# Performance work log

Hardware: AMD Instinct MI355X
Metric: run time of the kernel (lower is better)

The kernel has to match this reference:

```python
import jax, jax.numpy as jnp
from jax import lax
import numpy as np

B, C_IN, C_OUT, H, W, K = 4, 128, 256, 64, 64, 3
KK = K * K
MID = C_IN // 4
EPS = 1e-5


def conv2d(x, w, b, pad, groups=1):
    out = lax.conv_general_dilated(x, w, (1, 1), [(pad, pad), (pad, pad)],
                                   feature_group_count=groups,
                                   dimension_numbers=('NCHW', 'OIHW', 'NCHW'))
    return out + b[None, :, None, None]


def bnorm(x, g, b, m, v):
    # inference-mode BatchNorm2d
    scale = (g / jnp.sqrt(v + EPS))
    return (x - m[None, :, None, None]) * scale[None, :, None, None] + b[None, :, None, None]


def bilinear_gather(x, py, px):
    # x: (B,C,H,W); py/px: (B,KK,H,W) float sample coords; zero outside bounds
    Bb, C, Hh, Ww = x.shape
    xf = x.reshape(Bb, C, Hh * Ww)
    y0 = jnp.floor(py)
    x0 = jnp.floor(px)
    wy1 = py - y0
    wx1 = px - x0

    def corner(yc, xc, wgt):
        valid = (yc >= 0) & (yc <= Hh - 1) & (xc >= 0) & (xc <= Ww - 1)
        yi = jnp.clip(yc, 0, Hh - 1).astype(jnp.int32)
        xi = jnp.clip(xc, 0, Ww - 1).astype(jnp.int32)
        idx = (yi * Ww + xi).reshape(Bb, -1)  # (B, KK*H*W)
        g = jax.vmap(lambda f, i: f[:, i])(xf, idx).reshape(Bb, C, *py.shape[1:])
        return g * (wgt * valid)[:, None]

    return (corner(y0, x0, (1 - wy1) * (1 - wx1))
            + corner(y0, x0 + 1, (1 - wy1) * wx1)
            + corner(y0 + 1, x0, wy1 * (1 - wx1))
            + corner(y0 + 1, x0 + 1, wy1 * wx1))


def deform_conv2d(x, offset, mask, w, b, pad=1):
    # modulated deformable conv v2, stride=1, dilation=1, groups=1, dg=1
    Bb, C, Hh, Ww = x.shape
    off = offset.reshape(Bb, KK, 2, Hh, Ww)  # (dy,dx) per kernel point
    k = jnp.arange(KK)
    ky = (k // K).astype(x.dtype)
    kx = (k % K).astype(x.dtype)
    py = (jnp.arange(Hh, dtype=x.dtype) - pad)[None, None, :, None] + ky[None, :, None, None] + off[:, :, 0]
    px = (jnp.arange(Ww, dtype=x.dtype) - pad)[None, None, None, :] + kx[None, :, None, None] + off[:, :, 1]
    val = bilinear_gather(x, py, px) * mask[:, None]  # (B,C,KK,H,W)
    return jnp.einsum('bckhw,ock->bohw', val, w.reshape(w.shape[0], C, KK)) + b[None, :, None, None]


def setup_inputs() -> dict:
    key = jax.random.key(0)
    ks = iter(jax.random.split(key, 40))

    def P(shape, scale=0.05):
        return jax.random.normal(next(ks), shape, jnp.float32) * scale

    d = {}
    d['x'] = jax.random.normal(next(ks), (B, C_IN, H, W), jnp.float32)
    # DCConv offset branch
    d['oc1_w'] = P((MID, C_IN, 3, 3)); d['oc1_b'] = P((MID,))
    d['obn_g'] = jnp.ones((MID,)); d['obn_b'] = jnp.zeros((MID,))
    d['obn_m'] = jnp.zeros((MID,)); d['obn_v'] = jnp.ones((MID,))
    d['oc2_w'] = P((2 * KK, MID, 3, 3), 0.01); d['oc2_b'] = P((2 * KK,), 0.01)
    # DCConv mask branch
    d['mc1_w'] = P((MID, C_IN, 3, 3)); d['mc1_b'] = P((MID,))
    d['mbn_g'] = jnp.ones((MID,)); d['mbn_b'] = jnp.zeros((MID,))
    d['mbn_m'] = jnp.zeros((MID,)); d['mbn_v'] = jnp.ones((MID,))
    d['mc2_w'] = P((KK, MID, 3, 3), 0.01); d['mc2_b'] = jnp.ones((KK,))
    # DCConv main weight
    d['dc_w'] = P((C_OUT, C_IN, 3, 3)); d['dc_b'] = jnp.zeros((C_OUT,))
    # contour branch: depthwise 3x3 + BN + ReLU + 1x1
    d['cb_dw_w'] = P((C_IN, 1, 3, 3)); d['cb_dw_b'] = P((C_IN,))
    d['cbn_g'] = jnp.ones((C_IN,)); d['cbn_b'] = jnp.zeros((C_IN,))
    d['cbn_m'] = jnp.zeros((C_IN,)); d['cbn_v'] = jnp.ones((C_IN,))
    d['cb_pw_w'] = P((C_OUT // 2, C_IN, 1, 1)); d['cb_pw_b'] = P((C_OUT // 2,))
    # spatial attention 7x7 -> 1 channel
    d['sa_w'] = P((1, C_OUT + C_OUT // 2, 7, 7)); d['sa_b'] = jnp.zeros((1,))
    # fusion 1x1 + BN + ReLU
    d['fu_w'] = P((C_OUT, C_OUT + C_OUT // 2, 1, 1)); d['fu_b'] = jnp.zeros((C_OUT,))
    d['fbn_g'] = jnp.ones((C_OUT,)); d['fbn_b'] = jnp.zeros((C_OUT,))
    d['fbn_m'] = jnp.zeros((C_OUT,)); d['fbn_v'] = jnp.ones((C_OUT,))
    return d


def reference(x, oc1_w, oc1_b, obn_g, obn_b, obn_m, obn_v, oc2_w, oc2_b,
              mc1_w, mc1_b, mbn_g, mbn_b, mbn_m, mbn_v, mc2_w, mc2_b,
              dc_w, dc_b, cb_dw_w, cb_dw_b, cbn_g, cbn_b, cbn_m, cbn_v,
              cb_pw_w, cb_pw_b, sa_w, sa_b, fu_w, fu_b, fbn_g, fbn_b, fbn_m, fbn_v):
    # DCConv: offsets + sigmoid masks + modulated deformable conv
    h = jax.nn.relu(bnorm(conv2d(x, oc1_w, oc1_b, 1), obn_g, obn_b, obn_m, obn_v))
    offset = conv2d(h, oc2_w, oc2_b, 1)
    hm = jax.nn.relu(bnorm(conv2d(x, mc1_w, mc1_b, 1), mbn_g, mbn_b, mbn_m, mbn_v))
    mask = jax.nn.sigmoid(conv2d(hm, mc2_w, mc2_b, 1))
    main_feat = deform_conv2d(x, offset, mask, dc_w, dc_b, pad=1)
    # contour branch
    hc = jax.nn.relu(bnorm(conv2d(x, cb_dw_w, cb_dw_b, 1, groups=C_IN), cbn_g, cbn_b, cbn_m, cbn_v))
    contour_feat = conv2d(hc, cb_pw_w, cb_pw_b, 0)
    combined = jnp.concatenate([main_feat, contour_feat], axis=1)
    attn = jax.nn.sigmoid(conv2d(combined, sa_w, sa_b, 3))
    combined = combined * attn
    return jax.nn.relu(bnorm(conv2d(combined, fu_w, fu_b, 0), fbn_g, fbn_b, fbn_m, fbn_v))
```

## Files before the change

### kernel.cpp

```cpp
#include <hip/hip_runtime.h>
#include <hip/hip_bf16.h>
#include <math.h>

#define BN   4
#define CIN  128
#define COUT 256
#define HWP  4096

typedef __hip_bfloat16 bf16;
typedef __attribute__((ext_vector_type(8))) short sh8;
typedef __attribute__((ext_vector_type(4))) float f32x4;

__device__ __forceinline__ float b2f(bf16 v) { return __bfloat162float(v); }
__device__ __forceinline__ float bflo(unsigned u) { return __uint_as_float(u << 16); }
__device__ __forceinline__ float bfhi(unsigned u) { return __uint_as_float(u & 0xffff0000u); }
__device__ __forceinline__ unsigned short f2bfbits(float f) {
    union { bf16 h; unsigned short u; } cv; cv.h = __float2bfloat16(f); return cv.u;
}
__device__ __forceinline__ float bfj(const uint4& c, int j) {
    unsigned u = (&c.x)[j >> 1];
    return (j & 1) ? bfhi(u) : bflo(u);
}

__global__ __launch_bounds__(256) void transpose_x_kernel(const float* __restrict__ x,
                                                          bf16* __restrict__ xt)
{
    __shared__ bf16 t[64][136];
    const int b = blockIdx.x >> 6, chunk = blockIdx.x & 63;
    const int pos0 = chunk * 64;
    const int tid = threadIdx.x;
    const int lane = tid & 63, wv = tid >> 6;
    const float* xb = x + (size_t)b * CIN * HWP + pos0 + lane;
    #pragma unroll 4
    for (int j = 0; j < 32; j++) {
        int ci = wv * 32 + j;
        t[lane][ci] = __float2bfloat16(xb[(size_t)ci * HWP]);
    }
    __syncthreads();
    const int p = tid >> 2, cig = tid & 3;
    uint4* dst = (uint4*)(xt + ((size_t)b * HWP + pos0 + p) * 128 + cig * 32);
    const uint4* src = (const uint4*)&t[p][cig * 32];
    #pragma unroll
    for (int q = 0; q < 4; q++) dst[q] = src[q];
}

__global__ __launch_bounds__(256) void prep_wBf_kernel(const float* __restrict__ w,
                                                       bf16* __restrict__ wBf) {
    int o = blockIdx.x * 256 + threadIdx.x;
    if (o >= 256 * 1152) return;
    int j = o & 7, o2 = o >> 3;
    int lane = o2 & 63, t = o2 >> 6;
    int l16 = lane & 15, quad = lane >> 4;
    int mt = t & 3, t2 = t >> 2;
    int kt = t2 % 36, wv = t2 / 36;
    int co = wv * 64 + mt * 16 + l16;
    int kk = kt * 32 + quad * 8 + j;
    int k = kk >> 7, ci = kk & 127;
    wBf[o] = __float2bfloat16(w[co * 1152 + ci * 9 + k]);
}

__global__ __launch_bounds__(256) void prep_conv1_kernel(
    const float* __restrict__ oc1_w, const float* __restrict__ oc1_b,
    const float* __restrict__ obn_g, const float* __restrict__ obn_b,
    const float* __restrict__ obn_m, const float* __restrict__ obn_v,
    const float* __restrict__ mc1_w, const float* __restrict__ mc1_b,
    const float* __restrict__ mbn_g, const float* __restrict__ mbn_b,
    const float* __restrict__ mbn_m, const float* __restrict__ mbn_v,
    bf16* __restrict__ wCf, float* __restrict__ ab)
{
    int o = blockIdx.x * 256 + threadIdx.x;
    if (o < 64 * 1152) {
        int j = o & 7, o2 = o >> 3;
        int lane = o2 & 63, t = o2 >> 6;
        int l16 = lane & 15, quad = lane >> 4;
        int kt = t % 36, wv = t / 36;
        int co = wv * 16 + l16;
        int kk = kt * 32 + quad * 8 + j;
        int k = kk >> 7, ci = kk & 127;
        float v = (co < 32) ? oc1_w[co * 1152 + ci * 9 + k]
                            : mc1_w[(co - 32) * 1152 + ci * 9 + k];
        wCf[o] = __float2bfloat16(v);
    } else if (o < 64 * 1152 + 64) {
        int c = o - 64 * 1152;
        float g, bb, m, vv, bias;
        if (c < 32) { g = obn_g[c]; bb = obn_b[c]; m = obn_m[c]; vv = obn_v[c]; bias = oc1_b[c]; }
        else { int c2 = c - 32; g = mbn_g[c2]; bb = mbn_b[c2]; m = mbn_m[c2]; vv = mbn_v[c2]; bias = mc1_b[c2]; }
        float alpha = g / sqrtf(vv + 1e-5f);
        ab[c] = alpha;
        ab[64 + c] = (bias - m) * alpha + bb;
    }
}

__global__ __launch_bounds__(256) void prep_fuse_kernel(
    const float* __restrict__ fu_w, const float* __restrict__ fu_b,
    const float* __restrict__ fbn_g, const float* __restrict__ fbn_b,
    const float* __restrict__ fbn_m, const float* __restrict__ fbn_v,
    const float* __restrict__ sa_w,
    bf16* __restrict__ wFf, bf16* __restrict__ wSAf, float* __restrict__ fab)
{
    int o = blockIdx.x * 256 + threadIdx.x;
    if (o < 98304) {
        int j = o & 7, o2 = o >> 3;
        int lane = o2 & 63, t = o2 >> 6;
        int l16 = lane & 15, quad = lane >> 4;
        int mt = t & 3, t2 = t >> 2;
        int kt = t2 % 12, wv = t2 / 12;
        int co = wv * 64 + mt * 16 + l16;
        int kk = kt * 32 + quad * 8 + j;
        wFf[o] = __float2bfloat16(fu_w[co * 384 + kk]);
    } else if (o < 98304 + 24576) {
        int idx = o - 98304;
        int j = idx & 7, o2 = idx >> 3;
        int lane = o2 & 63, t = o2 >> 6;
        int l16 = lane & 15, quad = lane >> 4;
        int kt = t % 12, wv = t / 12;
        int jr = wv * 16 + l16;
        int kk = kt * 32 + quad * 8 + j;
        wSAf[idx] = (jr < 49) ? __float2bfloat16(sa_w[kk * 49 + jr]) : __float2bfloat16(0.f);
    } else if (o < 98304 + 24576 + 256) {
        int co = o - 98304 - 24576;
        float alpha = fbn_g[co] / sqrtf(fbn_v[co] + 1e-5f);
        fab[co] = alpha;
        fab[256 + co] = (fu_b[co] - fbn_m[co]) * alpha + fbn_b[co];
    }
}

__global__ __launch_bounds__(256) void prep_misc_kernel(
    const float* __restrict__ oc2_w, const float* __restrict__ mc2_w,
    const float* __restrict__ cb_pw_w,
    const float* __restrict__ cb_dw_b, const float* __restrict__ cbn_g,
    const float* __restrict__ cbn_b, const float* __restrict__ cbn_m,
    const float* __restrict__ cbn_v,
    bf16* __restrict__ wDf, bf16* __restrict__ wPf, float* __restrict__ dwab)
{
    int o = blockIdx.x * 256 + threadIdx.x;
    if (o < 18432) {
        int j = o & 7, o2 = o >> 3;
        int lane = o2 & 63, t = o2 >> 6;
        int l16 = lane & 15, quad = lane >> 4;
        int mt = t & 1, kt = t >> 1;
        int co = mt * 16 + l16;
        int kk = kt * 32 + quad * 8 + j;
        int k = kk >> 6, c = kk & 63;
        float v = 0.f;
        if (co < 18 && c < 32) v = oc2_w[co * 288 + c * 9 + k];
        else if (co >= 18 && co < 27 && c >= 32) v = mc2_w[(co - 18) * 288 + (c - 32) * 9 + k];
        wDf[o] = __float2bfloat16(v);
    } else if (o < 18432 + 16384) {
        int idx = o - 18432;
        int j = idx & 7, o2 = idx >> 3;
        int lane = o2 & 63, t = o2 >> 6;
        int l16 = lane & 15, quad = lane >> 4;
        int wv = t >> 3, kt = (t >> 1) & 3, mt = t & 1;
        int co = wv * 32 + mt * 16 + l16;
        int kk = kt * 32 + quad * 8 + j;
        wPf[idx] = __float2bfloat16(cb_pw_w[co * 128 + kk]);
    } else if (o < 18432 + 16384 + 128) {
        int c = o - 18432 - 16384;
        float alpha = cbn_g[c] / sqrtf(cbn_v[c] + 1e-5f);
        dwab[c] = alpha;
        dwab[128 + c] = (cb_dw_b[c] - cbn_m[c]) * alpha + cbn_b[c];
    }
}

__global__ __launch_bounds__(256) void conv1_mfma_kernel(
    const bf16* __restrict__ xt, const bf16* __restrict__ wCf, const float* __restrict__ ab,
    bf16* __restrict__ ht)
{
    __shared__ __align__(16) bf16 val[16][1160];

    const int bid = blockIdx.x;
    const int b = (bid & 7) >> 1;
    const int tile = ((bid >> 3) << 1) | (bid & 1);
    const int pos0 = tile * 16;
    const int y = tile >> 2, x0 = (tile & 3) * 16;
    const int tid = threadIdx.x;
    const int cig = tid & 15, pix = tid >> 4;
    const int ci0 = cig * 8;
    const int xxp = x0 + pix;

    const bf16* xtb = xt + (size_t)b * HWP * 128;
    #pragma unroll
    for (int k = 0; k < 9; k++) {
        int yy = y + k / 3 - 1, xx = xxp + k % 3 - 1;
        bool valid = (yy >= 0 && yy <= 63 && xx >= 0 && xx <= 63);
        uint4 c = {0, 0, 0, 0};
        if (valid) c = *(const uint4*)(xtb + (size_t)(yy * 64 + xx) * 128 + ci0);
        *(uint4*)&val[pix][k * 128 + ci0] = c;
    }
    __syncthreads();

    const int lane = tid & 63, wv = tid >> 6;
    const int quad = lane >> 4, l16 = lane & 15;
    f32x4 acc = {0, 0, 0, 0};
    const bf16* wl0 = wCf + (size_t)wv * 36 * 512 + lane * 8;
    const bf16* vbase = &val[l16][quad * 8];

    sh8 af = *(const sh8*)(wl0);
    sh8 bf = *(const sh8*)(vbase);
    sh8 afn, bfn;
    for (int kt = 0; kt < 36; kt++) {
        if (kt < 35) {
            afn = *(const sh8*)(wl0 + (kt + 1) * 512);
            bfn = *(const sh8*)(vbase + (kt + 1) * 32);
        }
        acc = __builtin_amdgcn_mfma_f32_16x16x32_bf16(af, bf, acc, 0, 0, 0);
        af = afn; bf = bfn;
    }

    float o0 = fmaxf(acc[0] * ab[wv * 16 + quad * 4 + 0] + ab[64 + wv * 16 + quad * 4 + 0], 0.f);
    float o1 = fmaxf(acc[1] * ab[wv * 16 + quad * 4 + 1] + ab[64 + wv * 16 + quad * 4 + 1], 0.f);
    float o2 = fmaxf(acc[2] * ab[wv * 16 + quad * 4 + 2] + ab[64 + wv * 16 + quad * 4 + 2], 0.f);
    float o3 = fmaxf(acc[3] * ab[wv * 16 + quad * 4 + 3] + ab[64 + wv * 16 + quad * 4 + 3], 0.f);
    uint2 pk;
    pk.x = (unsigned)f2bfbits(o0) | ((unsigned)f2bfbits(o1) << 16);
    pk.y = (unsigned)f2bfbits(o2) | ((unsigned)f2bfbits(o3) << 16);
    *(uint2*)(ht + ((size_t)b * HWP + pos0 + l16) * 64 + wv * 16 + quad * 4) = pk;
}

__global__ __launch_bounds__(256) void conv2_mfma_kernel(
    const bf16* __restrict__ ht, const bf16* __restrict__ wDf,
    const float* __restrict__ oc2_b, const float* __restrict__ mc2_b,
    float* __restrict__ offsb, float* __restrict__ mskb)
{
    __shared__ __align__(16) bf16 val[32][584];

    const int bid = blockIdx.x;
    const int b = bid >> 7, tile = bid & 127;
    const int y = tile >> 1, x0 = (tile & 1) * 32;
    const int tid = threadIdx.x;

    {
        const int cig = tid & 7, pix = tid >> 3;
        const int xxp = x0 + pix;
        const bf16* hb = ht + (size_t)b * HWP * 64;
        #pragma unroll
        for (int k = 0; k < 9; k++) {
            int yy = y + k / 3 - 1, xx = xxp + k % 3 - 1;
            bool valid = (yy >= 0 && yy <= 63 && xx >= 0 && xx <= 63);
            uint4 c = {0, 0, 0, 0};
            if (valid) c = *(const uint4*)(hb + (size_t)(yy * 64 + xx) * 64 + cig * 8);
            *(uint4*)&val[pix][k * 64 + cig * 8] = c;
        }
    }
    __syncthreads();

    const int lane = tid & 63, wv = tid >> 6;
    const int quad = lane >> 4, l16 = lane & 15;
    const int ph = wv >> 1, mt = wv & 1;
    f32x4 acc = {0, 0, 0, 0};
    const bf16* wl0 = wDf + ((size_t)mt * 64 + lane) * 8;
    const bf16* vbase = &val[ph * 16 + l16][quad * 8];

    sh8 af = *(const sh8*)(wl0);
    sh8 bf = *(const sh8*)(vbase);
    sh8 afn, bfn;
    for (int kt = 0; kt < 18; kt++) {
        if (kt < 17) {
            afn = *(const sh8*)(wl0 + (kt + 1) * 1024);
            bfn = *(const sh8*)(vbase + (kt + 1) * 32);
        }
        acc = __builtin_amdgcn_mfma_f32_16x16x32_bf16(af, bf, acc, 0, 0, 0);
        af = afn; bf = bfn;
    }

    const int pos = y * 64 + x0 + ph * 16 + l16;
    #pragma unroll
    for (int r = 0; r < 4; r++) {
        int co = mt * 16 + quad * 4 + r;
        if (co < 18) {
            offsb[(size_t)(b * 18 + co) * HWP + pos] = acc[r] + oc2_b[co];
        } else if (co < 27) {
            float s = acc[r] + mc2_b[co - 18];
            mskb[(size_t)(b * 9 + (co - 18)) * HWP + pos] = 1.f / (1.f + expf(-s));
        }
    }
}

__global__ __launch_bounds__(256) void dwconv_px_kernel(
    const bf16* __restrict__ xt, const float* __restrict__ dw_w, const float* __restrict__ dwab,
    bf16* __restrict__ htc)
{
    __shared__ float wl[1152];
    __shared__ float abl[256];
    const int bid = blockIdx.x;
    const int b = bid >> 8, tile = bid & 255;
    const int y = tile >> 2, x0 = (tile & 3) * 16;
    const int tid = threadIdx.x;
    for (int i = tid; i < 1152; i += 256) wl[i] = dw_w[i];
    if (tid < 256) abl[tid] = dwab[tid];
    __syncthreads();

    const int cig = tid & 15, pix = tid >> 4;
    const int ci0 = cig * 8;
    const int xxp = x0 + pix;
    const bf16* xtb = xt + (size_t)b * HWP * 128;

    float g[8] = {0, 0, 0, 0, 0, 0, 0, 0};
    #pragma unroll
    for (int k = 0; k < 9; k++) {
        int yy = y + k / 3 - 1, xx = xxp + k % 3 - 1;
        if (yy < 0 || yy > 63 || xx < 0 || xx > 63) continue;
        uint4 c = *(const uint4*)(xtb + (size_t)(yy * 64 + xx) * 128 + ci0);
        #pragma unroll
        for (int j = 0; j < 8; j++)
            g[j] += wl[(ci0 + j) * 9 + k] * bfj(c, j);
    }
    float o[8];
    #pragma unroll
    for (int j = 0; j < 8; j++)
        o[j] = fmaxf(g[j] * abl[ci0 + j] + abl[128 + ci0 + j], 0.f);
    uint4 pk;
    pk.x = (unsigned)f2bfbits(o[0]) | ((unsigned)f2bfbits(o[1]) << 16);
    pk.y = (unsigned)f2bfbits(o[2]) | ((unsigned)f2bfbits(o[3]) << 16);
    pk.z = (unsigned)f2bfbits(o[4]) | ((unsigned)f2bfbits(o[5]) << 16);
    pk.w = (unsigned)f2bfbits(o[6]) | ((unsigned)f2bfbits(o[7]) << 16);
    *(uint4*)(htc + ((size_t)b * HWP + y * 64 + xxp) * 128 + ci0) = pk;
}

__global__ __launch_bounds__(256) void pw_mfma_kernel(
    const bf16* __restrict__ htc, const bf16* __restrict__ wPf, const float* __restrict__ bias,
    bf16* __restrict__ combined)
{
    const int bid = blockIdx.x;
    const int b = bid >> 8, tile = bid & 255;
    const int pos0 = tile * 16;
    const int tid = threadIdx.x;
    const int lane = tid & 63, wv = tid >> 6;
    const int quad = lane >> 4, l16 = lane & 15;

    f32x4 acc[2] = {f32x4{0,0,0,0}, f32x4{0,0,0,0}};
    const bf16* fb = htc + ((size_t)b * HWP + pos0 + l16) * 128 + quad * 8;
    const bf16* wl0 = wPf + (size_t)wv * 4096 + lane * 8;
    for (int kt = 0; kt < 4; kt++) {
        sh8 bf = *(const sh8*)(fb + kt * 32);
        #pragma unroll
        for (int mt = 0; mt < 2; mt++) {
            sh8 af = *(const sh8*)(wl0 + (kt * 2 + mt) * 512);
            acc[mt] = __builtin_amdgcn_mfma_f32_16x16x32_bf16(af, bf, acc[mt], 0, 0, 0);
        }
    }

    bf16* ct = combined + ((size_t)b * HWP + pos0 + l16) * 384 + 256;
    #pragma unroll
    for (int mt = 0; mt < 2; mt++) {
        int co_b = wv * 32 + mt * 16 + quad * 4;
        uint2 pk;
        pk.x = (unsigned)f2bfbits(acc[mt][0] + bias[co_b])     | ((unsigned)f2bfbits(acc[mt][1] + bias[co_b + 1]) << 16);
        pk.y = (unsigned)f2bfbits(acc[mt][2] + bias[co_b + 2]) | ((unsigned)f2bfbits(acc[mt][3] + bias[co_b + 3]) << 16);
        *(uint2*)(ct + co_b) = pk;
    }
}

__global__ __launch_bounds__(256) void deform_kernel(
    const bf16* __restrict__ xt, const float* __restrict__ offs, const float* __restrict__ msk,
    const bf16* __restrict__ wBf, const float* __restrict__ bias, bf16* __restrict__ combined)
{
    __shared__ __align__(16) bf16 val[16][1160];
    __shared__ int   ti[144][4];
    __shared__ float tw[144][4];

    const int bid = blockIdx.x;
    const int b = (bid & 7) >> 1;
    const int tile = ((bid >> 3) << 1) | (bid & 1);
    const int pos0 = tile * 16;
    const int tid = threadIdx.x;

    if (tid < 144) {
        int k = tid >> 4, pix = tid & 15;
        int pos = pos0 + pix;
        int y = pos >> 6, xc = pos & 63;
        float offy = offs[(size_t)(b * 18 + 2 * k) * HWP + pos];
        float offx = offs[(size_t)(b * 18 + 2 * k + 1) * HWP + pos];
        float m = msk[(size_t)(b * 9 + k) * HWP + pos];
        float py = (float)(y - 1 + k / 3) + offy;
        float px = (float)(xc - 1 + k % 3) + offx;
        float fy = floorf(py), fx = floorf(px);
        float wy1 = py - fy, wx1 = px - fx;
        int y0 = (int)fy, x0 = (int)fx;
        int y1 = y0 + 1, x1 = x0 + 1;
        bool vy0 = (y0 >= 0 && y0 <= 63), vy1 = (y1 >= 0 && y1 <= 63);
        bool vx0 = (x0 >= 0 && x0 <= 63), vx1 = (x1 >= 0 && x1 <= 63);
        int cy0 = min(max(y0, 0), 63), cy1 = min(max(y1, 0), 63);
        int cx0 = min(max(x0, 0), 63), cx1 = min(max(x1, 0), 63);
        ti[tid][0] = cy0 * 64 + cx0;  tw[tid][0] = (vy0 && vx0) ? (1.f - wy1) * (1.f - wx1) * m : 0.f;
        ti[tid][1] = cy0 * 64 + cx1;  tw[tid][1] = (vy0 && vx1) ? (1.f - wy1) * wx1 * m : 0.f;
        ti[tid][2] = cy1 * 64 + cx0;  tw[tid][2] = (vy1 && vx0) ? wy1 * (1.f - wx1) * m : 0.f;
        ti[tid][3] = cy1 * 64 + cx1;  tw[tid][3] = (vy1 && vx1) ? wy1 * wx1 * m : 0.f;
    }
    __syncthreads();

    {
        const int cig = tid & 15, pix = tid >> 4;
        const int ci0 = cig * 8;
        const bf16* xtb = xt + (size_t)b * HWP * 128;
        for (int k = 0; k < 9; k++) {
            const int e = k * 16 + pix;
            const int i0 = ti[e][0], i1 = ti[e][1], i2 = ti[e][2], i3 = ti[e][3];
            const float w0 = tw[e][0], w1 = tw[e][1], w2 = tw[e][2], w3 = tw[e][3];
            uint4 c0 = *(const uint4*)(xtb + (size_t)i0 * 128 + ci0);
            uint4 c1 = *(const uint4*)(xtb + (size_t)i1 * 128 + ci0);
            uint4 c2 = *(const uint4*)(xtb + (size_t)i2 * 128 + ci0);
            uint4 c3 = *(const uint4*)(xtb + (size_t)i3 * 128 + ci0);
            float g[8];
            #pragma unroll
            for (int j = 0; j < 8; j++)
                g[j] = w0 * bfj(c0, j) + w1 * bfj(c1, j) + w2 * bfj(c2, j) + w3 * bfj(c3, j);
            uint4 pk;
            pk.x = (unsigned)f2bfbits(g[0]) | ((unsigned)f2bfbits(g[1]) << 16);
            pk.y = (unsigned)f2bfbits(g[2]) | ((unsigned)f2bfbits(g[3]) << 16);
            pk.z = (unsigned)f2bfbits(g[4]) | ((unsigned)f2bfbits(g[5]) << 16);
            pk.w = (unsigned)f2bfbits(g[6]) | ((unsigned)f2bfbits(g[7]) << 16);
            *(uint4*)&val[pix][k * 128 + ci0] = pk;
        }
    }
    __syncthreads();

    const int lane = tid & 63, wv = tid >> 6;
    const int quad = lane >> 4, l16 = lane & 15;
    f32x4 acc[4] = {f32x4{0,0,0,0}, f32x4{0,0,0,0}, f32x4{0,0,0,0}, f32x4{0,0,0,0}};

    const bf16* wl0 = wBf + (size_t)wv * 73728 + lane * 8;
    const bf16* vbase = &val[l16][quad * 8];

    sh8 af[4], afn[4], bf, bfn;
    bf = *(const sh8*)(vbase);
    #pragma unroll
    for (int mt = 0; mt < 4; mt++) af[mt] = *(const sh8*)(wl0 + mt * 512);
    for (int kt = 0; kt < 36; kt++) {
        if (kt < 35) {
            bfn = *(const sh8*)(vbase + (kt + 1) * 32);
            #pragma unroll
            for (int mt = 0; mt < 4; mt++)
                afn[mt] = *(const sh8*)(wl0 + ((kt + 1) * 4 + mt) * 512);
        }
        #pragma unroll
        for (int mt = 0; mt < 4; mt++)
            acc[mt] = __builtin_amdgcn_mfma_f32_16x16x32_bf16(af[mt], bf, acc[mt], 0, 0, 0);
        bf = bfn;
        #pragma unroll
        for (int mt = 0; mt < 4; mt++) af[mt] = afn[mt];
    }

    bf16* ct = combined + ((size_t)b * HWP + pos0 + l16) * 384;
    #pragma unroll
    for (int mt = 0; mt < 4; mt++) {
        int co_b = wv * 64 + mt * 16 + quad * 4;
        uint2 pk;
        pk.x = (unsigned)f2bfbits(acc[mt][0] + bias[co_b])     | ((unsigned)f2bfbits(acc[mt][1] + bias[co_b + 1]) << 16);
        pk.y = (unsigned)f2bfbits(acc[mt][2] + bias[co_b + 2]) | ((unsigned)f2bfbits(acc[mt][3] + bias[co_b + 3]) << 16);
        *(uint2*)(ct + co_b) = pk;
    }
}

__global__ __launch_bounds__(256) void sa_gemm_kernel(
    const bf16* __restrict__ combined, const bf16* __restrict__ wSAf, float* __restrict__ part)
{
    const int bid = blockIdx.x;
    const int b = bid >> 8, tile = bid & 255;
    const int pos0 = tile * 16;
    const int tid = threadIdx.x;
    const int lane = tid & 63, wv = tid >> 6;
    const int quad = lane >> 4, l16 = lane & 15;

    f32x4 acc = {0, 0, 0, 0};
    const bf16* fb = combined + ((size_t)b * HWP + pos0 + l16) * 384 + quad * 8;
    const bf16* wl0 = wSAf + (size_t)wv * 6144 + lane * 8;

    sh8 af = *(const sh8*)(wl0);
    sh8 bf = *(const sh8*)(fb);
    sh8 afn, bfn;
    for (int kt = 0; kt < 12; kt++) {
        if (kt < 11) {
            afn = *(const sh8*)(wl0 + (kt + 1) * 512);
            bfn = *(const sh8*)(fb + (kt + 1) * 32);
        }
        acc = __builtin_amdgcn_mfma_f32_16x16x32_bf16(af, bf, acc, 0, 0, 0);
        af = afn; bf = bfn;
    }
    #pragma unroll
    for (int r = 0; r < 4; r++) {
        int j = wv * 16 + quad * 4 + r;
        if (j < 49) part[(size_t)(j * BN + b) * HWP + pos0 + l16] = acc[r];
    }
}

__global__ __launch_bounds__(256) void attn_fin_kernel(
    const float* __restrict__ part, const float* __restrict__ sa_b, float* __restrict__ attn)
{
    int i = blockIdx.x * 256 + threadIdx.x;
    if (i >= BN * HWP) return;
    int b = i >> 12, pos = i & 4095;
    int y = pos >> 6, x = pos & 63;
    float s = sa_b[0];
    #pragma unroll
    for (int j = 0; j < 49; j++) {
        int yy = y + j / 7 - 3, xx = x + j % 7 - 3;
        if (yy < 0 || yy > 63 || xx < 0 || xx > 63) continue;
        s += part[(size_t)(j * BN + b) * HWP + yy * 64 + xx];
    }
    attn[i] = 1.f / (1.f + expf(-s));
}

__global__ __launch_bounds__(256) void fuse_kernel(
    const bf16* __restrict__ combined, const float* __restrict__ attn,
    const bf16* __restrict__ wFf, const float* __restrict__ fab, float* __restrict__ out)
{
    const int bid = blockIdx.x;
    const int b = bid >> 8, tile = bid & 255;
    const int pos0 = tile * 16;
    const int tid = threadIdx.x;
    const int lane = tid & 63, wv = tid >> 6;
    const int quad = lane >> 4, l16 = lane & 15;

    f32x4 acc[4] = {f32x4{0,0,0,0}, f32x4{0,0,0,0}, f32x4{0,0,0,0}, f32x4{0,0,0,0}};
    const bf16* fb = combined + ((size_t)b * HWP + pos0 + l16) * 384 + quad * 8;
    const bf16* wl0 = wFf + (size_t)wv * 24576 + lane * 8;

    sh8 af[4], afn[4], bf, bfn;
    bf = *(const sh8*)(fb);
    #pragma unroll
    for (int mt = 0; mt < 4; mt++) af[mt] = *(const sh8*)(wl0 + mt * 512);
    for (int kt = 0; kt < 12; kt++) {
        if (kt < 11) {
            bfn = *(const sh8*)(fb + (kt + 1) * 32);
            #pragma unroll
            for (int mt = 0; mt < 4; mt++)
                afn[mt] = *(const sh8*)(wl0 + ((kt + 1) * 4 + mt) * 512);
        }
        #pragma unroll
        for (int mt = 0; mt < 4; mt++)
            acc[mt] = __builtin_amdgcn_mfma_f32_16x16x32_bf16(af[mt], bf, acc[mt], 0, 0, 0);
        bf = bfn;
        #pragma unroll
        for (int mt = 0; mt < 4; mt++) af[mt] = afn[mt];
    }

    float a = attn[(size_t)b * HWP + pos0 + l16];
    float* op = out + (size_t)b * COUT * HWP + pos0 + l16;
    #pragma unroll
    for (int mt = 0; mt < 4; mt++) {
        int co_b = wv * 64 + mt * 16 + quad * 4;
        #pragma unroll
        for (int r = 0; r < 4; r++) {
            int co = co_b + r;
            float o = fmaxf(acc[mt][r] * a * fab[co] + fab[256 + co], 0.f);
            op[(size_t)co * HWP] = o;
        }
    }
}

extern "C" void kernel_launch(void* const* d_in, const int* in_sizes, int n_in,
                              void* d_out, int out_size, void* d_ws, size_t ws_size,
                              hipStream_t stream)
{
    const float* x      = (const float*)d_in[0];
    const float* oc1_w  = (const float*)d_in[1];
    const float* oc1_b  = (const float*)d_in[2];
    const float* obn_g  = (const float*)d_in[3];
    const float* obn_b  = (const float*)d_in[4];
    const float* obn_m  = (const float*)d_in[5];
    const float* obn_v  = (const float*)d_in[6];
    const float* oc2_w  = (const float*)d_in[7];
    const float* oc2_b  = (const float*)d_in[8];
    const float* mc1_w  = (const float*)d_in[9];
    const float* mc1_b  = (const float*)d_in[10];
    const float* mbn_g  = (const float*)d_in[11];
    const float* mbn_b  = (const float*)d_in[12];
    const float* mbn_m  = (const float*)d_in[13];
    const float* mbn_v  = (const float*)d_in[14];
    const float* mc2_w  = (const float*)d_in[15];
    const float* mc2_b  = (const float*)d_in[16];
    const float* dc_w   = (const float*)d_in[17];
    const float* dc_b   = (const float*)d_in[18];
    const float* cb_dw_w= (const float*)d_in[19];
    const float* cb_dw_b= (const float*)d_in[20];
    const float* cbn_g  = (const float*)d_in[21];
    const float* cbn_b  = (const float*)d_in[22];
    const float* cbn_m  = (const float*)d_in[23];
    const float* cbn_v  = (const float*)d_in[24];
    const float* cb_pw_w= (const float*)d_in[25];
    const float* cb_pw_b= (const float*)d_in[26];
    const float* sa_w   = (const float*)d_in[27];
    const float* sa_b   = (const float*)d_in[28];
    const float* fu_w   = (const float*)d_in[29];
    const float* fu_b   = (const float*)d_in[30];
    const float* fbn_g  = (const float*)d_in[31];
    const float* fbn_b  = (const float*)d_in[32];
    const float* fbn_m  = (const float*)d_in[33];
    const float* fbn_v  = (const float*)d_in[34];

    bf16*  ht    = (bf16*)d_ws;
    bf16*  htc   = ht + 1048576;
    float* offsb = (float*)(htc + 2097152);
    float* mskb  = offsb + 294912;
    bf16*  comb  = (bf16*)(mskb + 147456);
    float* part  = (float*)(comb + 6291456);
    float* attn  = part + 802816;
    bf16*  xt    = (bf16*)(attn + 16384);
    bf16*  wBf   = xt + 2097152;
    bf16*  wCf   = wBf + 294912;
    float* ab    = (float*)(wCf + 73728);
    bf16*  wFf   = (bf16*)(ab + 128);
    bf16*  wSAf  = wFf + 98304;
    float* fab   = (float*)(wSAf + 24576);
    bf16*  wDf   = (bf16*)(fab + 512);
    bf16*  wPf   = wDf + 18432;
    float* dwab  = (float*)(wPf + 16384);

    float* out = (float*)d_out;

    transpose_x_kernel<<<256, 256, 0, stream>>>(x, xt);
    prep_wBf_kernel<<<1152, 256, 0, stream>>>(dc_w, wBf);
    prep_conv1_kernel<<<289, 256, 0, stream>>>(oc1_w, oc1_b, obn_g, obn_b, obn_m, obn_v,
                                               mc1_w, mc1_b, mbn_g, mbn_b, mbn_m, mbn_v, wCf, ab);
    prep_fuse_kernel<<<482, 256, 0, stream>>>(fu_w, fu_b, fbn_g, fbn_b, fbn_m, fbn_v, sa_w,
                                              wFf, wSAf, fab);
    prep_misc_kernel<<<137, 256, 0, stream>>>(oc2_w, mc2_w, cb_pw_w,
                                              cb_dw_b, cbn_g, cbn_b, cbn_m, cbn_v,
                                              wDf, wPf, dwab);
    conv1_mfma_kernel<<<1024, 256, 0, stream>>>(xt, wCf, ab, ht);
    conv2_mfma_kernel<<<512, 256, 0, stream>>>(ht, wDf, oc2_b, mc2_b, offsb, mskb);
    dwconv_px_kernel<<<1024, 256, 0, stream>>>(xt, cb_dw_w, dwab, htc);
    pw_mfma_kernel<<<1024, 256, 0, stream>>>(htc, wPf, cb_pw_b, comb);
    deform_kernel<<<1024, 256, 0, stream>>>(xt, offsb, mskb, wBf, dc_b, comb);
    sa_gemm_kernel<<<1024, 256, 0, stream>>>(comb, wSAf, part);
    attn_fin_kernel<<<64, 256, 0, stream>>>(part, sa_b, attn);
    fuse_kernel<<<1024, 256, 0, stream>>>(comb, attn, wFf, fab, out);
}
```

Baseline: 237.6 us.

## Merge prep kernels, fuse depthwise+pointwise and attention-finalize, retile deform to 32 pixels

Merges the four weight-prep kernels into one launch. Fuses the depthwise conv into the pointwise MFMA kernel through shared memory, and folds the attention-finalize reduction into the fuse kernel. Together these remove launches and the round-trips of the htc and attn intermediates through global memory. The deform kernel now handles 32 pixels per block in two channel halves, so each weight fragment is reused across two MFMA column tiles, at the cost of an extra barrier and half as many blocks.

Result: faster. 212.9 us (-10.4%).

```diff
diff --git a/kernel.cpp b/kernel.cpp
--- a/kernel.cpp
+++ b/kernel.cpp
@@ -44,33 +44,42 @@
     for (int q = 0; q < 4; q++) dst[q] = src[q];
 }
 
-__global__ __launch_bounds__(256) void prep_wBf_kernel(const float* __restrict__ w,
-                                                       bf16* __restrict__ wBf) {
-    int o = blockIdx.x * 256 + threadIdx.x;
-    if (o >= 256 * 1152) return;
-    int j = o & 7, o2 = o >> 3;
-    int lane = o2 & 63, t = o2 >> 6;
-    int l16 = lane & 15, quad = lane >> 4;
-    int mt = t & 3, t2 = t >> 2;
-    int kt = t2 % 36, wv = t2 / 36;
-    int co = wv * 64 + mt * 16 + l16;
-    int kk = kt * 32 + quad * 8 + j;
-    int k = kk >> 7, ci = kk & 127;
-    wBf[o] = __float2bfloat16(w[co * 1152 + ci * 9 + k]);
-}
-
-__global__ __launch_bounds__(256) void prep_conv1_kernel(
+__global__ __launch_bounds__(256) void prep_all_kernel(
+    const float* __restrict__ dc_w,
     const float* __restrict__ oc1_w, const float* __restrict__ oc1_b,
     const float* __restrict__ obn_g, const float* __restrict__ obn_b,
     const float* __restrict__ obn_m, const float* __restrict__ obn_v,
     const float* __restrict__ mc1_w, const float* __restrict__ mc1_b,
     const float* __restrict__ mbn_g, const float* __restrict__ mbn_b,
     const float* __restrict__ mbn_m, const float* __restrict__ mbn_v,
-    bf16* __restrict__ wCf, float* __restrict__ ab)
+    const float* __restrict__ fu_w, const float* __restrict__ fu_b,
+    const float* __restrict__ fbn_g, const float* __restrict__ fbn_b,
+    const float* __restrict__ fbn_m, const float* __restrict__ fbn_v,
+    const float* __restrict__ sa_w,
+    const float* __restrict__ oc2_w, const float* __restrict__ mc2_w,
+    const float* __restrict__ cb_pw_w,
+    const float* __restrict__ cb_dw_b, const float* __restrict__ cbn_g,
+    const float* __restrict__ cbn_b, const float* __restrict__ cbn_m,
+    const float* __restrict__ cbn_v,
+    bf16* __restrict__ wBf2, bf16* __restrict__ wCf, float* __restrict__ ab,
+    bf16* __restrict__ wFf, bf16* __restrict__ wSAf, float* __restrict__ fab,
+    bf16* __restrict__ wDf, bf16* __restrict__ wPf, float* __restrict__ dwab)
 {
     int o = blockIdx.x * 256 + threadIdx.x;
-    if (o < 64 * 1152) {
+    if (o < 294912) {
         int j = o & 7, o2 = o >> 3;
+        int lane = o2 & 63, t = o2 >> 6;
+        int l16 = lane & 15, quad = lane >> 4;
+        int mt = t & 3, t2 = t >> 2;
+        int kt = t2 % 18, t3 = t2 / 18;
+        int h = t3 & 1, wv = t3 >> 1;
+        int co = wv * 64 + mt * 16 + l16;
+        int kkh = kt * 32 + quad * 8 + j;
+        int k = kkh >> 6, ci = h * 64 + (kkh & 63);
+        wBf2[o] = __float2bfloat16(dc_w[co * 1152 + ci * 9 + k]);
+    } else if (o < 368640) {
+        int idx = o - 294912;
+        int j = idx & 7, o2 = idx >> 3;
         int lane = o2 & 63, t = o2 >> 6;
         int l16 = lane & 15, quad = lane >> 4;
         int kt = t % 36, wv = t / 36;
@@ -79,37 +88,27 @@
         int k = kk >> 7, ci = kk & 127;
         float v = (co < 32) ? oc1_w[co * 1152 + ci * 9 + k]
                             : mc1_w[(co - 32) * 1152 + ci * 9 + k];
-        wCf[o] = __float2bfloat16(v);
-    } else if (o < 64 * 1152 + 64) {
-        int c = o - 64 * 1152;
+        wCf[idx] = __float2bfloat16(v);
+    } else if (o < 368704) {
+        int c = o - 368640;
         float g, bb, m, vv, bias;
         if (c < 32) { g = obn_g[c]; bb = obn_b[c]; m = obn_m[c]; vv = obn_v[c]; bias = oc1_b[c]; }
         else { int c2 = c - 32; g = mbn_g[c2]; bb = mbn_b[c2]; m = mbn_m[c2]; vv = mbn_v[c2]; bias = mc1_b[c2]; }
         float alpha = g / sqrtf(vv + 1e-5f);
         ab[c] = alpha;
         ab[64 + c] = (bias - m) * alpha + bb;
-    }
-}
-
-__global__ __launch_bounds__(256) void prep_fuse_kernel(
-    const float* __restrict__ fu_w, const float* __restrict__ fu_b,
-    const float* __restrict__ fbn_g, const float* __restrict__ fbn_b,
-    const float* __restrict__ fbn_m, const float* __restrict__ fbn_v,
-    const float* __restrict__ sa_w,
-    bf16* __restrict__ wFf, bf16* __restrict__ wSAf, float* __restrict__ fab)
-{
-    int o = blockIdx.x * 256 + threadIdx.x;
-    if (o < 98304) {
-        int j = o & 7, o2 = o >> 3;
+    } else if (o < 467008) {
+        int idx = o - 368704;
+        int j = idx & 7, o2 = idx >> 3;
         int lane = o2 & 63, t = o2 >> 6;
         int l16 = lane & 15, quad = lane >> 4;
         int mt = t & 3, t2 = t >> 2;
         int kt = t2 % 12, wv = t2 / 12;
         int co = wv * 64 + mt * 16 + l16;
         int kk = kt * 32 + quad * 8 + j;
-        wFf[o] = __float2bfloat16(fu_w[co * 384 + kk]);
-    } else if (o < 98304 + 24576) {
-        int idx = o - 98304;
+        wFf[idx] = __float2bfloat16(fu_w[co * 384 + kk]);
+    } else if (o < 491584) {
+        int idx = o - 467008;
         int j = idx & 7, o2 = idx >> 3;
         int lane = o2 & 63, t = o2 >> 6;
         int l16 = lane & 15, quad = lane >> 4;
@@ -117,25 +116,14 @@
         int jr = wv * 16 + l16;
         int kk = kt * 32 + quad * 8 + j;
         wSAf[idx] = (jr < 49) ? __float2bfloat16(sa_w[kk * 49 + jr]) : __float2bfloat16(0.f);
-    } else if (o < 98304 + 24576 + 256) {
-        int co = o - 98304 - 24576;
+    } else if (o < 491840) {
+        int co = o - 491584;
         float alpha = fbn_g[co] / sqrtf(fbn_v[co] + 1e-5f);
         fab[co] = alpha;
         fab[256 + co] = (fu_b[co] - fbn_m[co]) * alpha + fbn_b[co];
-    }
-}
-
-__global__ __launch_bounds__(256) void prep_misc_kernel(
-    const float* __restrict__ oc2_w, const float* __restrict__ mc2_w,
-    const float* __restrict__ cb_pw_w,
-    const float* __restrict__ cb_dw_b, const float* __restrict__ cbn_g,
-    const float* __restrict__ cbn_b, const float* __restrict__ cbn_m,
-    const float* __restrict__ cbn_v,
-    bf16* __restrict__ wDf, bf16* __restrict__ wPf, float* __restrict__ dwab)
-{
-    int o = blockIdx.x * 256 + threadIdx.x;
-    if (o < 18432) {
-        int j = o & 7, o2 = o >> 3;
+    } else if (o < 510272) {
+        int idx = o - 491840;
+        int j = idx & 7, o2 = idx >> 3;
         int lane = o2 & 63, t = o2 >> 6;
         int l16 = lane & 15, quad = lane >> 4;
         int mt = t & 1, kt = t >> 1;
@@ -145,9 +133,9 @@
         float v = 0.f;
         if (co < 18 && c < 32) v = oc2_w[co * 288 + c * 9 + k];
         else if (co >= 18 && co < 27 && c >= 32) v = mc2_w[(co - 18) * 288 + (c - 32) * 9 + k];
-        wDf[o] = __float2bfloat16(v);
-    } else if (o < 18432 + 16384) {
-        int idx = o - 18432;
+        wDf[idx] = __float2bfloat16(v);
+    } else if (o < 526656) {
+        int idx = o - 510272;
         int j = idx & 7, o2 = idx >> 3;
         int lane = o2 & 63, t = o2 >> 6;
         int l16 = lane & 15, quad = lane >> 4;
@@ -155,8 +143,8 @@
         int co = wv * 32 + mt * 16 + l16;
         int kk = kt * 32 + quad * 8 + j;
         wPf[idx] = __float2bfloat16(cb_pw_w[co * 128 + kk]);
-    } else if (o < 18432 + 16384 + 128) {
-        int c = o - 18432 - 16384;
+    } else if (o < 526784) {
+        int c = o - 526656;
         float alpha = cbn_g[c] / sqrtf(cbn_v[c] + 1e-5f);
         dwab[c] = alpha;
         dwab[128 + c] = (cb_dw_b[c] - cbn_m[c]) * alpha + cbn_b[c];
@@ -277,61 +265,56 @@
     }
 }
 
-__global__ __launch_bounds__(256) void dwconv_px_kernel(
+__global__ __launch_bounds__(256) void dwpw_kernel(
     const bf16* __restrict__ xt, const float* __restrict__ dw_w, const float* __restrict__ dwab,
-    bf16* __restrict__ htc)
+    const bf16* __restrict__ wPf, const float* __restrict__ pw_b, bf16* __restrict__ combined)
 {
     __shared__ float wl[1152];
     __shared__ float abl[256];
+    __shared__ __align__(16) bf16 vdw[16][136];
     const int bid = blockIdx.x;
     const int b = bid >> 8, tile = bid & 255;
+    const int pos0 = tile * 16;
     const int y = tile >> 2, x0 = (tile & 3) * 16;
     const int tid = threadIdx.x;
     for (int i = tid; i < 1152; i += 256) wl[i] = dw_w[i];
-    if (tid < 256) abl[tid] = dwab[tid];
-    __syncthreads();
-
-    const int cig = tid & 15, pix = tid >> 4;
-    const int ci0 = cig * 8;
-    const int xxp = x0 + pix;
-    const bf16* xtb = xt + (size_t)b * HWP * 128;
-
-    float g[8] = {0, 0, 0, 0, 0, 0, 0, 0};
-    #pragma unroll
-    for (int k = 0; k < 9; k++) {
-        int yy = y + k / 3 - 1, xx = xxp + k % 3 - 1;
-        if (yy < 0 || yy > 63 || xx < 0 || xx > 63) continue;
-        uint4 c = *(const uint4*)(xtb + (size_t)(yy * 64 + xx) * 128 + ci0);
+    abl[tid] = dwab[tid];
+    __syncthreads();
+
+    {
+        const int cig = tid & 15, pix = tid >> 4;
+        const int ci0 = cig * 8;
+        const int xxp = x0 + pix;
+        const bf16* xtb = xt + (size_t)b * HWP * 128;
+        float g[8] = {0, 0, 0, 0, 0, 0, 0, 0};
+        #pragma unroll
+        for (int k = 0; k < 9; k++) {
+            int yy = y + k / 3 - 1, xx = xxp + k % 3 - 1;
+            if (yy < 0 || yy > 63 || xx < 0 || xx > 63) continue;
+            uint4 c = *(const uint4*)(xtb + (size_t)(yy * 64 + xx) * 128 + ci0);
+            #pragma unroll
+            for (int j = 0; j < 8; j++)
+                g[j] += wl[(ci0 + j) * 9 + k] * bfj(c, j);
+        }
+        uint4 pk;
+        float o[8];
         #pragma unroll
         for (int j = 0; j < 8; j++)
-            g[j] += wl[(ci0 + j) * 9 + k] * bfj(c, j);
-    }
-    float o[8];
-    #pragma unroll
-    for (int j = 0; j < 8; j++)
-        o[j] = fmaxf(g[j] * abl[ci0 + j] + abl[128 + ci0 + j], 0.f);
-    uint4 pk;
-    pk.x = (unsigned)f2bfbits(o[0]) | ((unsigned)f2bfbits(o[1]) << 16);
-    pk.y = (unsigned)f2bfbits(o[2]) | ((unsigned)f2bfbits(o[3]) << 16);
-    pk.z = (unsigned)f2bfbits(o[4]) | ((unsigned)f2bfbits(o[5]) << 16);
-    pk.w = (unsigned)f2bfbits(o[6]) | ((unsigned)f2bfbits(o[7]) << 16);
-    *(uint4*)(htc + ((size_t)b * HWP + y * 64 + xxp) * 128 + ci0) = pk;
-}
-
-__global__ __launch_bounds__(256) void pw_mfma_kernel(
-    const bf16* __restrict__ htc, const bf16* __restrict__ wPf, const float* __restrict__ bias,
-    bf16* __restrict__ combined)
-{
-    const int bid = blockIdx.x;
-    const int b = bid >> 8, tile = bid & 255;
-    const int pos0 = tile * 16;
-    const int tid = threadIdx.x;
+            o[j] = fmaxf(g[j] * abl[ci0 + j] + abl[128 + ci0 + j], 0.f);
+        pk.x = (unsigned)f2bfbits(o[0]) | ((unsigned)f2bfbits(o[1]) << 16);
+        pk.y = (unsigned)f2bfbits(o[2]) | ((unsigned)f2bfbits(o[3]) << 16);
+        pk.z = (unsigned)f2bfbits(o[4]) | ((unsigned)f2bfbits(o[5]) << 16);
+        pk.w = (unsigned)f2bfbits(o[6]) | ((unsigned)f2bfbits(o[7]) << 16);
+        *(uint4*)&vdw[pix][ci0] = pk;
+    }
+    __syncthreads();
+
     const int lane = tid & 63, wv = tid >> 6;
     const int quad = lane >> 4, l16 = lane & 15;
-
     f32x4 acc[2] = {f32x4{0,0,0,0}, f32x4{0,0,0,0}};
-    const bf16* fb = htc + ((size_t)b * HWP + pos0 + l16) * 128 + quad * 8;
+    const bf16* fb = &vdw[l16][quad * 8];
     const bf16* wl0 = wPf + (size_t)wv * 4096 + lane * 8;
+    #pragma unroll
     for (int kt = 0; kt < 4; kt++) {
         sh8 bf = *(const sh8*)(fb + kt * 32);
         #pragma unroll
@@ -346,28 +329,28 @@
     for (int mt = 0; mt < 2; mt++) {
         int co_b = wv * 32 + mt * 16 + quad * 4;
         uint2 pk;
-        pk.x = (unsigned)f2bfbits(acc[mt][0] + bias[co_b])     | ((unsigned)f2bfbits(acc[mt][1] + bias[co_b + 1]) << 16);
-        pk.y = (unsigned)f2bfbits(acc[mt][2] + bias[co_b + 2]) | ((unsigned)f2bfbits(acc[mt][3] + bias[co_b + 3]) << 16);
+        pk.x = (unsigned)f2bfbits(acc[mt][0] + pw_b[co_b])     | ((unsigned)f2bfbits(acc[mt][1] + pw_b[co_b + 1]) << 16);
+        pk.y = (unsigned)f2bfbits(acc[mt][2] + pw_b[co_b + 2]) | ((unsigned)f2bfbits(acc[mt][3] + pw_b[co_b + 3]) << 16);
         *(uint2*)(ct + co_b) = pk;
     }
 }
 
 __global__ __launch_bounds__(256) void deform_kernel(
     const bf16* __restrict__ xt, const float* __restrict__ offs, const float* __restrict__ msk,
-    const bf16* __restrict__ wBf, const float* __restrict__ bias, bf16* __restrict__ combined)
-{
-    __shared__ __align__(16) bf16 val[16][1160];
-    __shared__ int   ti[144][4];
-    __shared__ float tw[144][4];
+    const bf16* __restrict__ wBf2, const float* __restrict__ bias, bf16* __restrict__ combined)
+{
+    __shared__ __align__(16) bf16 val[32][584];
+    __shared__ int   ti[288][4];
+    __shared__ float tw[288][4];
 
     const int bid = blockIdx.x;
     const int b = (bid & 7) >> 1;
     const int tile = ((bid >> 3) << 1) | (bid & 1);
-    const int pos0 = tile * 16;
+    const int pos0 = tile * 32;
     const int tid = threadIdx.x;
 
-    if (tid < 144) {
-        int k = tid >> 4, pix = tid & 15;
+    for (int e = tid; e < 288; e += 256) {
+        int k = e >> 5, pix = e & 31;
         int pos = pos0 + pix;
         int y = pos >> 6, xc = pos & 63;
         float offy = offs[(size_t)(b * 18 + 2 * k) * HWP + pos];
@@ -383,73 +366,82 @@
         bool vx0 = (x0 >= 0 && x0 <= 63), vx1 = (x1 >= 0 && x1 <= 63);
         int cy0 = min(max(y0, 0), 63), cy1 = min(max(y1, 0), 63);
         int cx0 = min(max(x0, 0), 63), cx1 = min(max(x1, 0), 63);
-        ti[tid][0] = cy0 * 64 + cx0;  tw[tid][0] = (vy0 && vx0) ? (1.f - wy1) * (1.f - wx1) * m : 0.f;
-        ti[tid][1] = cy0 * 64 + cx1;  tw[tid][1] = (vy0 && vx1) ? (1.f - wy1) * wx1 * m : 0.f;
-        ti[tid][2] = cy1 * 64 + cx0;  tw[tid][2] = (vy1 && vx0) ? wy1 * (1.f - wx1) * m : 0.f;
-        ti[tid][3] = cy1 * 64 + cx1;  tw[tid][3] = (vy1 && vx1) ? wy1 * wx1 * m : 0.f;
-    }
-    __syncthreads();
-
-    {
-        const int cig = tid & 15, pix = tid >> 4;
-        const int ci0 = cig * 8;
-        const bf16* xtb = xt + (size_t)b * HWP * 128;
-        for (int k = 0; k < 9; k++) {
-            const int e = k * 16 + pix;
-            const int i0 = ti[e][0], i1 = ti[e][1], i2 = ti[e][2], i3 = ti[e][3];
-            const float w0 = tw[e][0], w1 = tw[e][1], w2 = tw[e][2], w3 = tw[e][3];
-            uint4 c0 = *(const uint4*)(xtb + (size_t)i0 * 128 + ci0);
-            uint4 c1 = *(const uint4*)(xtb + (size_t)i1 * 128 + ci0);
-            uint4 c2 = *(const uint4*)(xtb + (size_t)i2 * 128 + ci0);
-            uint4 c3 = *(const uint4*)(xtb + (size_t)i3 * 128 + ci0);
-            float g[8];
-            #pragma unroll
-            for (int j = 0; j < 8; j++)
-                g[j] = w0 * bfj(c0, j) + w1 * bfj(c1, j) + w2 * bfj(c2, j) + w3 * bfj(c3, j);
-            uint4 pk;
-            pk.x = (unsigned)f2bfbits(g[0]) | ((unsigned)f2bfbits(g[1]) << 16);
-            pk.y = (unsigned)f2bfbits(g[2]) | ((unsigned)f2bfbits(g[3]) << 16);
-            pk.z = (unsigned)f2bfbits(g[4]) | ((unsigned)f2bfbits(g[5]) << 16);
-            pk.w = (unsigned)f2bfbits(g[6]) | ((unsigned)f2bfbits(g[7]) << 16);
-            *(uint4*)&val[pix][k * 128 + ci0] = pk;
-        }
+        ti[e][0] = cy0 * 64 + cx0;  tw[e][0] = (vy0 && vx0) ? (1.f - wy1) * (1.f - wx1) * m : 0.f;
+        ti[e][1] = cy0 * 64 + cx1;  tw[e][1] = (vy0 && vx1) ? (1.f - wy1) * wx1 * m : 0.f;
+        ti[e][2] = cy1 * 64 + cx0;  tw[e][2] = (vy1 && vx0) ? wy1 * (1.f - wx1) * m : 0.f;
+        ti[e][3] = cy1 * 64 + cx1;  tw[e][3] = (vy1 && vx1) ? wy1 * wx1 * m : 0.f;
     }
     __syncthreads();
 
     const int lane = tid & 63, wv = tid >> 6;
     const int quad = lane >> 4, l16 = lane & 15;
-    f32x4 acc[4] = {f32x4{0,0,0,0}, f32x4{0,0,0,0}, f32x4{0,0,0,0}, f32x4{0,0,0,0}};
-
-    const bf16* wl0 = wBf + (size_t)wv * 73728 + lane * 8;
-    const bf16* vbase = &val[l16][quad * 8];
-
-    sh8 af[4], afn[4], bf, bfn;
-    bf = *(const sh8*)(vbase);
-    #pragma unroll
-    for (int mt = 0; mt < 4; mt++) af[mt] = *(const sh8*)(wl0 + mt * 512);
-    for (int kt = 0; kt < 36; kt++) {
-        if (kt < 35) {
-            bfn = *(const sh8*)(vbase + (kt + 1) * 32);
+    f32x4 acc[4][2] = {{f32x4{0,0,0,0}, f32x4{0,0,0,0}}, {f32x4{0,0,0,0}, f32x4{0,0,0,0}},
+                       {f32x4{0,0,0,0}, f32x4{0,0,0,0}}, {f32x4{0,0,0,0}, f32x4{0,0,0,0}}};
+    const bf16* xtb = xt + (size_t)b * HWP * 128;
+
+    #pragma unroll
+    for (int h = 0; h < 2; h++) {
+        if (h) __syncthreads();
+        {
+            const int cig = tid & 7, pix = tid >> 3;
+            const int ci0 = h * 64 + cig * 8;
+            for (int k = 0; k < 9; k++) {
+                const int e = k * 32 + pix;
+                const int i0 = ti[e][0], i1 = ti[e][1], i2 = ti[e][2], i3 = ti[e][3];
+                const float w0 = tw[e][0], w1 = tw[e][1], w2 = tw[e][2], w3 = tw[e][3];
+                uint4 c0 = *(const uint4*)(xtb + (size_t)i0 * 128 + ci0);
+                uint4 c1 = *(const uint4*)(xtb + (size_t)i1 * 128 + ci0);
+                uint4 c2 = *(const uint4*)(xtb + (size_t)i2 * 128 + ci0);
+                uint4 c3 = *(const uint4*)(xtb + (size_t)i3 * 128 + ci0);
+                float g[8];
+                #pragma unroll
+                for (int j = 0; j < 8; j++)
+                    g[j] = w0 * bfj(c0, j) + w1 * bfj(c1, j) + w2 * bfj(c2, j) + w3 * bfj(c3, j);
+                uint4 pk;
+                pk.x = (unsigned)f2bfbits(g[0]) | ((unsigned)f2bfbits(g[1]) << 16);
+                pk.y = (unsigned)f2bfbits(g[2]) | ((unsigned)f2bfbits(g[3]) << 16);
+                pk.z = (unsigned)f2bfbits(g[4]) | ((unsigned)f2bfbits(g[5]) << 16);
+                pk.w = (unsigned)f2bfbits(g[6]) | ((unsigned)f2bfbits(g[7]) << 16);
+                *(uint4*)&val[pix][k * 64 + cig * 8] = pk;
+            }
+        }
+        __syncthreads();
+
+        const bf16* wl0 = wBf2 + ((size_t)(wv * 2 + h) * 72) * 512 + lane * 8;
+        const bf16* vb0 = &val[l16][quad * 8];
+        const bf16* vb1 = &val[16 + l16][quad * 8];
+        sh8 af[4], afn[4];
+        #pragma unroll
+        for (int mt = 0; mt < 4; mt++) af[mt] = *(const sh8*)(wl0 + mt * 512);
+        for (int kt = 0; kt < 18; kt++) {
+            sh8 b0 = *(const sh8*)(vb0 + kt * 32);
+            sh8 b1 = *(const sh8*)(vb1 + kt * 32);
+            if (kt < 17) {
+                #pragma unroll
+                for (int mt = 0; mt < 4; mt++)
+                    afn[mt] = *(const sh8*)(wl0 + ((kt + 1) * 4 + mt) * 512);
+            }
             #pragma unroll
-            for (int mt = 0; mt < 4; mt++)
-                afn[mt] = *(const sh8*)(wl0 + ((kt + 1) * 4 + mt) * 512);
-        }
-        #pragma unroll
-        for (int mt = 0; mt < 4; mt++)
-            acc[mt] = __builtin_amdgcn_mfma_f32_16x16x32_bf16(af[mt], bf, acc[mt], 0, 0, 0);
-        bf = bfn;
-        #pragma unroll
-        for (int mt = 0; mt < 4; mt++) af[mt] = afn[mt];
-    }
-
-    bf16* ct = combined + ((size_t)b * HWP + pos0 + l16) * 384;
-    #pragma unroll
-    for (int mt = 0; mt < 4; mt++) {
-        int co_b = wv * 64 + mt * 16 + quad * 4;
-        uint2 pk;
-        pk.x = (unsigned)f2bfbits(acc[mt][0] + bias[co_b])     | ((unsigned)f2bfbits(acc[mt][1] + bias[co_b + 1]) << 16);
-        pk.y = (unsigned)f2bfbits(acc[mt][2] + bias[co_b + 2]) | ((unsigned)f2bfbits(acc[mt][3] + bias[co_b + 3]) << 16);
-        *(uint2*)(ct + co_b) = pk;
+            for (int mt = 0; mt < 4; mt++) {
+                acc[mt][0] = __builtin_amdgcn_mfma_f32_16x16x32_bf16(af[mt], b0, acc[mt][0], 0, 0, 0);
+                acc[mt][1] = __builtin_amdgcn_mfma_f32_16x16x32_bf16(af[mt], b1, acc[mt][1], 0, 0, 0);
+            }
+            #pragma unroll
+            for (int mt = 0; mt < 4; mt++) af[mt] = afn[mt];
+        }
+    }
+
+    #pragma unroll
+    for (int ph = 0; ph < 2; ph++) {
+        bf16* ct = combined + ((size_t)b * HWP + pos0 + ph * 16 + l16) * 384;
+        #pragma unroll
+        for (int mt = 0; mt < 4; mt++) {
+            int co_b = wv * 64 + mt * 16 + quad * 4;
+            uint2 pk;
+            pk.x = (unsigned)f2bfbits(acc[mt][ph][0] + bias[co_b])     | ((unsigned)f2bfbits(acc[mt][ph][1] + bias[co_b + 1]) << 16);
+            pk.y = (unsigned)f2bfbits(acc[mt][ph][2] + bias[co_b + 2]) | ((unsigned)f2bfbits(acc[mt][ph][3] + bias[co_b + 3]) << 16);
+            *(uint2*)(ct + co_b) = pk;
+        }
     }
 }
 
@@ -485,31 +477,39 @@
     }
 }
 
-__global__ __launch_bounds__(256) void attn_fin_kernel(
-    const float* __restrict__ part, const float* __restrict__ sa_b, float* __restrict__ attn)
-{
-    int i = blockIdx.x * 256 + threadIdx.x;
-    if (i >= BN * HWP) return;
-    int b = i >> 12, pos = i & 4095;
-    int y = pos >> 6, x = pos & 63;
-    float s = sa_b[0];
-    #pragma unroll
-    for (int j = 0; j < 49; j++) {
-        int yy = y + j / 7 - 3, xx = x + j % 7 - 3;
-        if (yy < 0 || yy > 63 || xx < 0 || xx > 63) continue;
-        s += part[(size_t)(j * BN + b) * HWP + yy * 64 + xx];
-    }
-    attn[i] = 1.f / (1.f + expf(-s));
-}
-
 __global__ __launch_bounds__(256) void fuse_kernel(
-    const bf16* __restrict__ combined, const float* __restrict__ attn,
+    const bf16* __restrict__ combined, const float* __restrict__ part, const float* __restrict__ sa_b,
     const bf16* __restrict__ wFf, const float* __restrict__ fab, float* __restrict__ out)
 {
+    __shared__ float sattn[16][17];
+    __shared__ float lattn[16];
+
     const int bid = blockIdx.x;
     const int b = bid >> 8, tile = bid & 255;
     const int pos0 = tile * 16;
+    const int y = tile >> 2, x0 = (tile & 3) * 16;
     const int tid = threadIdx.x;
+
+    {
+        const int px = tid & 15, g = tid >> 4;
+        const int xp = x0 + px;
+        float s = 0.f;
+        for (int j = g; j < 49; j += 16) {
+            int yy = y + j / 7 - 3, xx = xp + j % 7 - 3;
+            if (yy < 0 || yy > 63 || xx < 0 || xx > 63) continue;
+            s += part[(size_t)(j * BN + b) * HWP + yy * 64 + xx];
+        }
+        sattn[px][g] = s;
+    }
+    __syncthreads();
+    if (tid < 16) {
+        float t = sa_b[0];
+        #pragma unroll
+        for (int g = 0; g < 16; g++) t += sattn[tid][g];
+        lattn[tid] = 1.f / (1.f + expf(-t));
+    }
+    __syncthreads();
+
     const int lane = tid & 63, wv = tid >> 6;
     const int quad = lane >> 4, l16 = lane & 15;
 
@@ -536,7 +536,7 @@
         for (int mt = 0; mt < 4; mt++) af[mt] = afn[mt];
     }
 
-    float a = attn[(size_t)b * HWP + pos0 + l16];
+    float a = lattn[l16];
     float* op = out + (size_t)b * COUT * HWP + pos0 + l16;
     #pragma unroll
     for (int mt = 0; mt < 4; mt++) {
@@ -591,15 +591,13 @@
     const float* fbn_v  = (const float*)d_in[34];
 
     bf16*  ht    = (bf16*)d_ws;
-    bf16*  htc   = ht + 1048576;
-    float* offsb = (float*)(htc + 2097152);
+    float* offsb = (float*)(ht + 1048576);
     float* mskb  = offsb + 294912;
     bf16*  comb  = (bf16*)(mskb + 147456);
     float* part  = (float*)(comb + 6291456);
-    float* attn  = part + 802816;
-    bf16*  xt    = (bf16*)(attn + 16384);
-    bf16*  wBf   = xt + 2097152;
-    bf16*  wCf   = wBf + 294912;
+    bf16*  xt    = (bf16*)(part + 802816);
+    bf16*  wBf2  = xt + 2097152;
+    bf16*  wCf   = wBf2 + 294912;
     float* ab    = (float*)(wCf + 73728);
     bf16*  wFf   = (bf16*)(ab + 128);
     bf16*  wSAf  = wFf + 98304;
@@ -611,20 +609,16 @@
     float* out = (float*)d_out;
 
     transpose_x_kernel<<<256, 256, 0, stream>>>(x, xt);
-    prep_wBf_kernel<<<1152, 256, 0, stream>>>(dc_w, wBf);
-    prep_conv1_kernel<<<289, 256, 0, stream>>>(oc1_w, oc1_b, obn_g, obn_b, obn_m, obn_v,
-                                               mc1_w, mc1_b, mbn_g, mbn_b, mbn_m, mbn_v, wCf, ab);
-    prep_fuse_kernel<<<482, 256, 0, stream>>>(fu_w, fu_b, fbn_g, fbn_b, fbn_m, fbn_v, sa_w,
-                                              wFf, wSAf, fab);
-    prep_misc_kernel<<<137, 256, 0, stream>>>(oc2_w, mc2_w, cb_pw_w,
-                                              cb_dw_b, cbn_g, cbn_b, cbn_m, cbn_v,
-                                              wDf, wPf, dwab);
+    prep_all_kernel<<<2058, 256, 0, stream>>>(
+        dc_w, oc1_w, oc1_b, obn_g, obn_b, obn_m, obn_v,
+        mc1_w, mc1_b, mbn_g, mbn_b, mbn_m, mbn_v,
+        fu_w, fu_b, fbn_g, fbn_b, fbn_m, fbn_v, sa_w,
+        oc2_w, mc2_w, cb_pw_w, cb_dw_b, cbn_g, cbn_b, cbn_m, cbn_v,
+        wBf2, wCf, ab, wFf, wSAf, fab, wDf, wPf, dwab);
     conv1_mfma_kernel<<<1024, 256, 0, stream>>>(xt, wCf, ab, ht);
     conv2_mfma_kernel<<<512, 256, 0, stream>>>(ht, wDf, oc2_b, mc2_b, offsb, mskb);
-    dwconv_px_kernel<<<1024, 256, 0, stream>>>(xt, cb_dw_w, dwab, htc);
-    pw_mfma_kernel<<<1024, 256, 0, stream>>>(htc, wPf, cb_pw_b, comb);
-    deform_kernel<<<1024, 256, 0, stream>>>(xt, offsb, mskb, wBf, dc_b, comb);
+    dwpw_kernel<<<1024, 256, 0, stream>>>(xt, cb_dw_w, dwab, wPf, cb_pw_b, comb);
+    deform_kernel<<<512, 256, 0, stream>>>(xt, offsb, mskb, wBf2, dc_b, comb);
     sa_gemm_kernel<<<1024, 256, 0, stream>>>(comb, wSAf, part);
-    attn_fin_kernel<<<64, 256, 0, stream>>>(part, sa_b, attn);
-    fuse_kernel<<<1024, 256, 0, stream>>>(comb, attn, wFf, fab, out);
-}
+    fuse_kernel<<<1024, 256, 0, stream>>>(comb, part, sa_b, wFf, fab, out);
+}
```
